# Kernel optimization log

Hardware: AMD Instinct MI355X
Metric: run time of the kernel (lower is better)

The kernel has to match this reference:

```python
import jax, jax.numpy as jnp
import numpy as np

N_NODES = 10000
N_EDGES = 320000
DIM = 256
NUM_HEADS = 8
HEAD_DIM = DIM // NUM_HEADS


def setup_inputs() -> dict:
    key = jax.random.key(0)
    ks = jax.random.split(key, 8)
    s = 1.0 / np.sqrt(DIM)
    x = jax.random.normal(ks[0], (N_NODES, DIM), dtype=jnp.float32)
    src = jax.random.randint(ks[1], (N_EDGES,), 0, N_NODES, dtype=jnp.int32)
    dst = jax.random.randint(ks[2], (N_EDGES,), 0, N_NODES, dtype=jnp.int32)
    Wq = jax.random.normal(ks[3], (DIM, DIM), dtype=jnp.float32) * s
    Wk = jax.random.normal(ks[4], (DIM, DIM), dtype=jnp.float32) * s
    Wv = jax.random.normal(ks[5], (DIM, DIM), dtype=jnp.float32) * s
    Wo = jax.random.normal(ks[6], (DIM, DIM), dtype=jnp.float32) * s
    z = jnp.zeros((DIM,), dtype=jnp.float32)
    return {"x": x, "src": src, "dst": dst,
            "Wq": Wq, "bq": z, "Wk": Wk, "bk": z,
            "Wv": Wv, "bv": z, "Wo": Wo, "bo": z}


def reference(x, src, dst, Wq, bq, Wk, bk, Wv, bv, Wo, bo):
    N = x.shape[0]
    # nn.Linear: y = x @ W.T + b
    q = (x @ Wq.T + bq).reshape(N, NUM_HEADS, HEAD_DIM)
    k = (x @ Wk.T + bk).reshape(N, NUM_HEADS, HEAD_DIM)
    v = (x @ Wv.T + bv).reshape(N, NUM_HEADS, HEAD_DIM)
    # u_dot_v: dot(q[src], k[dst]) per head -> [E, H]
    score = jnp.einsum('ehd,ehd->eh', q[src], k[dst]) / np.sqrt(HEAD_DIM).astype(np.float32)
    # Faithful to source: F.softmax(dim=1) on [E, H, 1] -> softmax over HEADS axis
    attn = jax.nn.softmax(score, axis=1)  # [E, H]
    # u_mul_e then sum-reduce onto destination nodes
    m = v[src] * attn[:, :, None]  # [E, H, HEAD_DIM]
    h = jax.ops.segment_sum(m, dst, num_segments=N).reshape(N, DIM)
    out = h @ Wo.T + bo
    # dropout p=0.0 -> identity
    return out
```

## Files before the change

kernel.cpp:

```cpp
#include <hip/hip_runtime.h>
#include <stdint.h>

#define N_NODES 10000
#define N_EDGES 320000
#define DIM 256
#define NRANGE 4
#define RANGE_DIV 2500
#define PAD_SLOTS 32
#define CNT_STRIDE 16

typedef _Float16 half8 __attribute__((ext_vector_type(8)));
typedef _Float16 half2t __attribute__((ext_vector_type(2)));
typedef float floatx4 __attribute__((ext_vector_type(4)));

#define QK_SCALE 0.17677669529663687f

typedef __attribute__((address_space(3))) uint32_t lds_u32;
typedef __attribute__((address_space(1))) const uint32_t glob_u32;
__device__ __forceinline__ void load16_lds(const _Float16* g, _Float16* l) {
  __builtin_amdgcn_global_load_lds((glob_u32*)g, (lds_u32*)l, 16, 0, 0);
}

__device__ __forceinline__ half8 cvt8s(const float4 a, const float4 b, float sc) {
  half8 o;
  o[0] = (_Float16)(a.x * sc); o[1] = (_Float16)(a.y * sc);
  o[2] = (_Float16)(a.z * sc); o[3] = (_Float16)(a.w * sc);
  o[4] = (_Float16)(b.x * sc); o[5] = (_Float16)(b.y * sc);
  o[6] = (_Float16)(b.z * sc); o[7] = (_Float16)(b.w * sc);
  return o;
}

__global__ void __launch_bounds__(256) prep_k(
    const float* __restrict__ x, const float* __restrict__ Wq,
    const float* __restrict__ Wk, const float* __restrict__ Wv,
    const float* __restrict__ Wo,
    _Float16* __restrict__ xh, _Float16* __restrict__ Wcat,
    _Float16* __restrict__ Woh, int* __restrict__ cntp) {
  int b = blockIdx.x;
  int t = threadIdx.x;
  if (b < 1250) {
    int i = b * 256 + t;
    const float4* p = (const float4*)x;
    ((half8*)xh)[i] = cvt8s(p[2 * i], p[2 * i + 1], 1.0f);
  } else if (b < 1378) {
    int bb = b - 1250;
    int w = bb >> 5;
    int i = (bb & 31) * 256 + t;
    const float* in = (w == 0) ? Wq : (w == 1) ? Wv : (w == 2) ? Wk : Wo;
    _Float16* out = (w < 3) ? (Wcat + (size_t)w * 65536) : Woh;
    float sc = (w == 0) ? QK_SCALE : 1.0f;
    const float4* p = (const float4*)in;
    ((half8*)out)[i] = cvt8s(p[2 * i], p[2 * i + 1], sc);
  } else {
    int idx = (b - 1378) * 256 + t;
#pragma unroll
    for (int k = 0; k < 16; ++k) {
      int j = idx + k * 10240;
      if (j < 160000) ((int4*)cntp)[j] = (int4){0, 0, 0, 0};
    }
  }
}

template <typename STORE>
__device__ __forceinline__ void gemm_tile32(
    _Float16* As, _Float16* Bs,
    const _Float16* __restrict__ A, const _Float16* __restrict__ B,
    int m0, int n0, int t, STORE&& store_fn) {
  int lane = t & 63;
  int wid = t >> 6;
  int l16 = lane & 15;
  int quad = lane >> 4;
  int wm = wid >> 1, wn = wid & 1;

  floatx4 acc[4][4];
#pragma unroll
  for (int i = 0; i < 4; ++i)
#pragma unroll
    for (int j = 0; j < 4; ++j) acc[i][j] = (floatx4){0.f, 0.f, 0.f, 0.f};

  auto stage = [&](int ks, int buf) {
#pragma unroll
    for (int i = 0; i < 2; ++i) {
      int idx = i * 4 + wid;
      int c = idx >> 1;
      int hh2 = idx & 1;
      int r = hh2 * 64 + lane;
      int ar = m0 + r;
      if (ar >= N_NODES) ar = N_NODES - 1;
      load16_lds(A + (size_t)ar * 256 + ks * 32 + c * 8,
                 &As[buf * 4096 + (c * 128 + hh2 * 64) * 8]);
      load16_lds(B + (size_t)(n0 + r) * 256 + ks * 32 + c * 8,
                 &Bs[buf * 4096 + (c * 128 + hh2 * 64) * 8]);
    }
  };

  stage(0, 0);
  __syncthreads();

  for (int ks = 0; ks < 8; ++ks) {
    int bsel = ks & 1;
    if (ks < 7) stage(ks + 1, 1 - bsel);
    half8 af[4], bf[4];
#pragma unroll
    for (int i = 0; i < 4; ++i) {
      af[i] = *(const half8*)&As[bsel * 4096 + (quad * 128 + wm * 64 + i * 16 + l16) * 8];
      bf[i] = *(const half8*)&Bs[bsel * 4096 + (quad * 128 + wn * 64 + i * 16 + l16) * 8];
    }
#pragma unroll
    for (int mi = 0; mi < 4; ++mi)
#pragma unroll
      for (int ni = 0; ni < 4; ++ni)
        acc[mi][ni] =
            __builtin_amdgcn_mfma_f32_16x16x32_f16(af[mi], bf[ni], acc[mi][ni], 0, 0, 0);
    __syncthreads();
  }

#pragma unroll
  for (int mi = 0; mi < 4; ++mi) {
#pragma unroll
    for (int ni = 0; ni < 4; ++ni) {
      int col = n0 + wn * 64 + ni * 16 + l16;
#pragma unroll
      for (int r = 0; r < 4; ++r) {
        int row = m0 + wm * 64 + mi * 16 + quad * 4 + r;
        if (row < N_NODES) store_fn(row, col, acc[mi][ni][r]);
      }
    }
  }
}

__global__ void __launch_bounds__(256) gemm0_scatter_k(
    const _Float16* __restrict__ A, const _Float16* __restrict__ B,
    const float* __restrict__ b0, const float* __restrict__ b1,
    const float* __restrict__ b2,
    _Float16* __restrict__ qv, _Float16* __restrict__ kh,
    const int* __restrict__ src, const int* __restrict__ dst,
    int* __restrict__ cntp, int* __restrict__ slist4) {
  __shared__ _Float16 As[8192];
  __shared__ _Float16 Bs[8192];
  int u = blockIdx.x;
  int t = threadIdx.x;

  if (u >= 474) {
    int e0 = (u - 474) * 582;
    int e1 = e0 + 582;
    if (e1 > N_EDGES) e1 = N_EDGES;
    for (int e = e0 + t; e < e1; e += 256) {
      int s = src[e];
      int r = s / RANGE_DIV;
      int cell = dst[e] * NRANGE + r;
      int pos = atomicAdd(&cntp[(size_t)cell * CNT_STRIDE], 1);
      if (pos < PAD_SLOTS) slist4[cell * PAD_SLOTS + pos] = s;
    }
    return;
  }

  int bx = u % 79, by = u / 79;
  gemm_tile32(As, Bs, A, B, bx * 128, by * 128, t,
              [&](int row, int col, float v) {
                float bias = (col < 256) ? b0[col] * QK_SCALE
                                         : (col < 512) ? b1[col - 256] : b2[col - 512];
                float val = v + bias;
                if (col < 512)
                  qv[(size_t)row * 512 + col] = (_Float16)val;
                else
                  kh[(size_t)row * 256 + (col - 512)] = (_Float16)val;
              });
}

__global__ void __launch_bounds__(256) gemm1_k(
    const _Float16* __restrict__ A, const _Float16* __restrict__ B,
    const float* __restrict__ b0, float* __restrict__ outf) {
  __shared__ _Float16 As[8192];
  __shared__ _Float16 Bs[8192];
  int t = threadIdx.x;
  gemm_tile32(As, Bs, A, B, blockIdx.x * 128, blockIdx.y * 128, t,
              [&](int row, int col, float v) {
                outf[(size_t)row * 256 + col] = v + b0[col];
              });
}

__global__ void __launch_bounds__(256, 4) aggregate_k(
    const _Float16* __restrict__ qv, const _Float16* __restrict__ kh,
    const int* __restrict__ slist4, const int* __restrict__ cntp,
    _Float16* __restrict__ hh) {
  int lane = threadIdx.x & 63;
  int n = blockIdx.x * 4 + (threadIdx.x >> 6);
  if (n >= N_NODES) return;
  int h = lane & 7;
  int g = lane >> 3;

  const int* cb = cntp + (size_t)n * (NRANGE * CNT_STRIDE);
  int d0 = min(cb[0 * CNT_STRIDE], PAD_SLOTS);
  int d1 = min(cb[1 * CNT_STRIDE], PAD_SLOTS);
  int d2 = min(cb[2 * CNT_STRIDE], PAD_SLOTS);
  int d3 = min(cb[3 * CNT_STRIDE], PAD_SLOTS);
  int o1 = d0, o2 = o1 + d1, o3 = o2 + d2;
  int T = o3 + d3;
  const int* nb = slist4 + (size_t)n * (NRANGE * PAD_SLOTS);

  int sidA = 0, sidB = 0;
  {
    int i0 = lane;
    int r0 = (i0 >= o1) + (i0 >= o2) + (i0 >= o3);
    int b0r = (r0 == 0) ? 0 : (r0 == 1) ? o1 : (r0 == 2) ? o2 : o3;
    if (i0 < T) sidA = nb[r0 * PAD_SLOTS + (i0 - b0r)];
    if (T > 64) {
      int i1 = lane + 64;
      int r1 = (i1 >= o1) + (i1 >= o2) + (i1 >= o3);
      int b1r = (r1 == 0) ? 0 : (r1 == 1) ? o1 : (r1 == 2) ? o2 : o3;
      if (i1 < T) sidB = nb[r1 * PAD_SLOTS + (i1 - b1r)];
    }
  }

  half8 kc[4];
  const half8* krow = (const half8*)(kh + (size_t)n * DIM + h * 32);
#pragma unroll
  for (int i = 0; i < 4; ++i) kc[i] = krow[i];
  const half2t* k2 = (const half2t*)kc;

  half2t acc[16];
#pragma unroll
  for (int i = 0; i < 16; ++i) acc[i] = (half2t){(_Float16)0.f, (_Float16)0.f};

  int iters = (T + 7) >> 3;
  if (iters > 0) {
    int s0 = __shfl(sidA, g);
    const half8* rr = (const half8*)(qv + (size_t)s0 * 512 + h * 32);
    half8 qc[4];
#pragma unroll
    for (int i = 0; i < 4; ++i) qc[i] = rr[i];
    bool valid = g < T;

#pragma unroll 1
    for (int jj = 0; jj < iters; ++jj) {
      half8 vc[4];
#pragma unroll
      for (int i = 0; i < 4; ++i) vc[i] = rr[32 + i];
      half8 nq[4];
      bool nvalid = false;
      const half8* nrr = rr;
      if (jj + 1 < iters) {
        int nidx = (jj + 1) * 8 + g;
        int ns = (jj + 1 < 8) ? __shfl(sidA, nidx) : __shfl(sidB, nidx - 64);
        nrr = (const half8*)(qv + (size_t)ns * 512 + h * 32);
#pragma unroll
        for (int i = 0; i < 4; ++i) nq[i] = nrr[i];
        nvalid = nidx < T;
      }
      const half2t* q2 = (const half2t*)qc;
      float pa = 0.f, pb = 0.f, pc = 0.f, pd = 0.f;
#pragma unroll
      for (int i = 0; i < 4; ++i) {
#if __has_builtin(__builtin_amdgcn_fdot2)
        pa = __builtin_amdgcn_fdot2(q2[i], k2[i], pa, false);
        pb = __builtin_amdgcn_fdot2(q2[4 + i], k2[4 + i], pb, false);
        pc = __builtin_amdgcn_fdot2(q2[8 + i], k2[8 + i], pc, false);
        pd = __builtin_amdgcn_fdot2(q2[12 + i], k2[12 + i], pd, false);
#else
        pa += (float)q2[i][0] * (float)k2[i][0] + (float)q2[i][1] * (float)k2[i][1];
        pb += (float)q2[4 + i][0] * (float)k2[4 + i][0] + (float)q2[4 + i][1] * (float)k2[4 + i][1];
        pc += (float)q2[8 + i][0] * (float)k2[8 + i][0] + (float)q2[8 + i][1] * (float)k2[8 + i][1];
        pd += (float)q2[12 + i][0] * (float)k2[12 + i][0] + (float)q2[12 + i][1] * (float)k2[12 + i][1];
#endif
      }
      float p = (pa + pb) + (pc + pd);
      float ex = __expf(p);
      float ssum = ex;
      ssum += __shfl_xor(ssum, 1);
      ssum += __shfl_xor(ssum, 2);
      ssum += __shfl_xor(ssum, 4);
      float a = valid ? (ex * __frcp_rn(ssum)) : 0.f;
      _Float16 ah = (_Float16)a;
      half2t ah2 = (half2t){ah, ah};
      const half2t* v2 = (const half2t*)vc;
#pragma unroll
      for (int i = 0; i < 16; ++i) acc[i] += v2[i] * ah2;
#pragma unroll
      for (int i = 0; i < 4; ++i) qc[i] = nq[i];
      rr = nrr;
      valid = nvalid;
    }
  }

#pragma unroll
  for (int i = 0; i < 16; ++i) {
    union { half2t h2; int v; } u;
    u.h2 = acc[i]; u.v = __shfl_xor(u.v, 8);  acc[i] += u.h2;
    u.h2 = acc[i]; u.v = __shfl_xor(u.v, 16); acc[i] += u.h2;
    u.h2 = acc[i]; u.v = __shfl_xor(u.v, 32); acc[i] += u.h2;
  }
  if (g == 0) {
    half8* hrow = (half8*)(hh + (size_t)n * DIM + h * 32);
    const half8* a8 = (const half8*)acc;
#pragma unroll
    for (int i = 0; i < 4; ++i) hrow[i] = a8[i];
  }
}

extern "C" void kernel_launch(void* const* d_in, const int* in_sizes, int n_in,
                              void* d_out, int out_size, void* d_ws, size_t ws_size,
                              hipStream_t stream) {
  const float* x = (const float*)d_in[0];
  const int* src = (const int*)d_in[1];
  const int* dst = (const int*)d_in[2];
  const float* Wq = (const float*)d_in[3];
  const float* bq = (const float*)d_in[4];
  const float* Wk = (const float*)d_in[5];
  const float* bk = (const float*)d_in[6];
  const float* Wv = (const float*)d_in[7];
  const float* bv = (const float*)d_in[8];
  const float* Wo = (const float*)d_in[9];
  const float* bo = (const float*)d_in[10];

  char* p = (char*)d_ws;
  const size_t SZ_NODE_H = (size_t)N_NODES * DIM * sizeof(_Float16);
  _Float16* xh = (_Float16*)p; p += SZ_NODE_H;
  _Float16* qvv = (_Float16*)p; p += 2 * SZ_NODE_H;
  _Float16* kh = (_Float16*)p; p += SZ_NODE_H;
  _Float16* hh = (_Float16*)p; p += SZ_NODE_H;
  _Float16* Wcat = (_Float16*)p; p += (size_t)768 * 256 * sizeof(_Float16);
  _Float16* Woh = (_Float16*)p; p += (size_t)256 * 256 * sizeof(_Float16);
  int* cntp = (int*)p; p += (size_t)N_NODES * NRANGE * CNT_STRIDE * sizeof(int);
  int* slist4 = (int*)p; p += (size_t)N_NODES * NRANGE * PAD_SLOTS * sizeof(int);

  prep_k<<<1418, 256, 0, stream>>>(x, Wq, Wk, Wv, Wo, xh, Wcat, Woh, cntp);

  gemm0_scatter_k<<<1024, 256, 0, stream>>>(xh, Wcat, bq, bv, bk, qvv, kh,
                                            src, dst, cntp, slist4);

  aggregate_k<<<2500, 256, 0, stream>>>(qvv, kh, slist4, cntp, hh);

  gemm1_k<<<dim3(79, 2), 256, 0, stream>>>(hh, Woh, bo, (float*)d_out);
}
```

Before: 168.9 us.

## Replace LDS-staged GEMM tiles with register-direct per-wave 32x64 MFMA tiles

The shared-memory double-buffered GEMM (global_load_lds plus block barriers) is replaced by a register-only scheme. Each wave loads its A and B fragments straight from global memory and prefetches the next k-step into registers. Tiles shrink from 128x128 per block to 128x64 per block, split as 32x64 per wave, which doubles the block count for both GEMMs and drops barriers and LDS use. The cost is lost operand reuse across waves, since each wave re-reads B from global/L2, and more total global traffic.

```diff
diff --git a/kernel.cpp b/kernel.cpp
--- a/kernel.cpp
+++ b/kernel.cpp
@@ -14,12 +14,6 @@
 typedef float floatx4 __attribute__((ext_vector_type(4)));
 
 #define QK_SCALE 0.17677669529663687f
-
-typedef __attribute__((address_space(3))) uint32_t lds_u32;
-typedef __attribute__((address_space(1))) const uint32_t glob_u32;
-__device__ __forceinline__ void load16_lds(const _Float16* g, _Float16* l) {
-  __builtin_amdgcn_global_load_lds((glob_u32*)g, (lds_u32*)l, 16, 0, 0);
-}
 
 __device__ __forceinline__ half8 cvt8s(const float4 a, const float4 b, float sc) {
   half8 o;
@@ -62,67 +56,64 @@
 }
 
 template <typename STORE>
-__device__ __forceinline__ void gemm_tile32(
-    _Float16* As, _Float16* Bs,
+__device__ __forceinline__ void gemm_reg(
     const _Float16* __restrict__ A, const _Float16* __restrict__ B,
-    int m0, int n0, int t, STORE&& store_fn) {
-  int lane = t & 63;
-  int wid = t >> 6;
+    int m0, int n0, int lane, STORE&& store_fn) {
   int l16 = lane & 15;
   int quad = lane >> 4;
-  int wm = wid >> 1, wn = wid & 1;
-
-  floatx4 acc[4][4];
-#pragma unroll
-  for (int i = 0; i < 4; ++i)
+
+  floatx4 acc[2][4];
+#pragma unroll
+  for (int i = 0; i < 2; ++i)
 #pragma unroll
     for (int j = 0; j < 4; ++j) acc[i][j] = (floatx4){0.f, 0.f, 0.f, 0.f};
 
-  auto stage = [&](int ks, int buf) {
-#pragma unroll
-    for (int i = 0; i < 2; ++i) {
-      int idx = i * 4 + wid;
-      int c = idx >> 1;
-      int hh2 = idx & 1;
-      int r = hh2 * 64 + lane;
-      int ar = m0 + r;
-      if (ar >= N_NODES) ar = N_NODES - 1;
-      load16_lds(A + (size_t)ar * 256 + ks * 32 + c * 8,
-                 &As[buf * 4096 + (c * 128 + hh2 * 64) * 8]);
-      load16_lds(B + (size_t)(n0 + r) * 256 + ks * 32 + c * 8,
-                 &Bs[buf * 4096 + (c * 128 + hh2 * 64) * 8]);
-    }
-  };
-
-  stage(0, 0);
-  __syncthreads();
-
+  const _Float16* ap[2];
+#pragma unroll
+  for (int mi = 0; mi < 2; ++mi) {
+    int r = m0 + mi * 16 + l16;
+    if (r >= N_NODES) r = N_NODES - 1;
+    ap[mi] = A + (size_t)r * 256 + quad * 8;
+  }
+  const _Float16* bp[4];
+#pragma unroll
+  for (int ni = 0; ni < 4; ++ni)
+    bp[ni] = B + (size_t)(n0 + ni * 16 + l16) * 256 + quad * 8;
+
+  half8 a0[2], b0[4], a1[2], b1[4];
+#pragma unroll
+  for (int mi = 0; mi < 2; ++mi) a0[mi] = *(const half8*)(ap[mi]);
+#pragma unroll
+  for (int ni = 0; ni < 4; ++ni) b0[ni] = *(const half8*)(bp[ni]);
+
+#pragma unroll
   for (int ks = 0; ks < 8; ++ks) {
-    int bsel = ks & 1;
-    if (ks < 7) stage(ks + 1, 1 - bsel);
-    half8 af[4], bf[4];
-#pragma unroll
-    for (int i = 0; i < 4; ++i) {
-      af[i] = *(const half8*)&As[bsel * 4096 + (quad * 128 + wm * 64 + i * 16 + l16) * 8];
-      bf[i] = *(const half8*)&Bs[bsel * 4096 + (quad * 128 + wn * 64 + i * 16 + l16) * 8];
-    }
-#pragma unroll
-    for (int mi = 0; mi < 4; ++mi)
+    if (ks < 7) {
+#pragma unroll
+      for (int mi = 0; mi < 2; ++mi) a1[mi] = *(const half8*)(ap[mi] + (ks + 1) * 32);
+#pragma unroll
+      for (int ni = 0; ni < 4; ++ni) b1[ni] = *(const half8*)(bp[ni] + (ks + 1) * 32);
+    }
+#pragma unroll
+    for (int mi = 0; mi < 2; ++mi)
 #pragma unroll
       for (int ni = 0; ni < 4; ++ni)
         acc[mi][ni] =
-            __builtin_amdgcn_mfma_f32_16x16x32_f16(af[mi], bf[ni], acc[mi][ni], 0, 0, 0);
-    __syncthreads();
-  }
-
-#pragma unroll
-  for (int mi = 0; mi < 4; ++mi) {
+            __builtin_amdgcn_mfma_f32_16x16x32_f16(a0[mi], b0[ni], acc[mi][ni], 0, 0, 0);
+#pragma unroll
+    for (int mi = 0; mi < 2; ++mi) a0[mi] = a1[mi];
+#pragma unroll
+    for (int ni = 0; ni < 4; ++ni) b0[ni] = b1[ni];
+  }
+
+#pragma unroll
+  for (int mi = 0; mi < 2; ++mi) {
 #pragma unroll
     for (int ni = 0; ni < 4; ++ni) {
-      int col = n0 + wn * 64 + ni * 16 + l16;
+      int col = n0 + ni * 16 + l16;
 #pragma unroll
       for (int r = 0; r < 4; ++r) {
-        int row = m0 + wm * 64 + mi * 16 + quad * 4 + r;
+        int row = m0 + mi * 16 + quad * 4 + r;
         if (row < N_NODES) store_fn(row, col, acc[mi][ni][r]);
       }
     }
@@ -136,13 +127,11 @@
     _Float16* __restrict__ qv, _Float16* __restrict__ kh,
     const int* __restrict__ src, const int* __restrict__ dst,
     int* __restrict__ cntp, int* __restrict__ slist4) {
-  __shared__ _Float16 As[8192];
-  __shared__ _Float16 Bs[8192];
   int u = blockIdx.x;
   int t = threadIdx.x;
 
-  if (u >= 474) {
-    int e0 = (u - 474) * 582;
+  if (u >= 948) {
+    int e0 = (u - 948) * 582;
     int e1 = e0 + 582;
     if (e1 > N_EDGES) e1 = N_EDGES;
     for (int e = e0 + t; e < e1; e += 256) {
@@ -156,28 +145,31 @@
   }
 
   int bx = u % 79, by = u / 79;
-  gemm_tile32(As, Bs, A, B, bx * 128, by * 128, t,
-              [&](int row, int col, float v) {
-                float bias = (col < 256) ? b0[col] * QK_SCALE
-                                         : (col < 512) ? b1[col - 256] : b2[col - 512];
-                float val = v + bias;
-                if (col < 512)
-                  qv[(size_t)row * 512 + col] = (_Float16)val;
-                else
-                  kh[(size_t)row * 256 + (col - 512)] = (_Float16)val;
-              });
+  int wid = t >> 6, lane = t & 63;
+  int m0 = bx * 128 + wid * 32;
+  int n0 = by * 64;
+  gemm_reg(A, B, m0, n0, lane,
+           [&](int row, int col, float v) {
+             float bias = (col < 256) ? b0[col] * QK_SCALE
+                                      : (col < 512) ? b1[col - 256] : b2[col - 512];
+             float val = v + bias;
+             if (col < 512)
+               qv[(size_t)row * 512 + col] = (_Float16)val;
+             else
+               kh[(size_t)row * 256 + (col - 512)] = (_Float16)val;
+           });
 }
 
 __global__ void __launch_bounds__(256) gemm1_k(
     const _Float16* __restrict__ A, const _Float16* __restrict__ B,
     const float* __restrict__ b0, float* __restrict__ outf) {
-  __shared__ _Float16 As[8192];
-  __shared__ _Float16 Bs[8192];
-  int t = threadIdx.x;
-  gemm_tile32(As, Bs, A, B, blockIdx.x * 128, blockIdx.y * 128, t,
-              [&](int row, int col, float v) {
-                outf[(size_t)row * 256 + col] = v + b0[col];
-              });
+  int u = blockIdx.x;
+  int bx = u % 79, by = u / 79;
+  int wid = threadIdx.x >> 6, lane = threadIdx.x & 63;
+  gemm_reg(A, B, bx * 128 + wid * 32, by * 64, lane,
+           [&](int row, int col, float v) {
+             outf[(size_t)row * 256 + col] = v + b0[col];
+           });
 }
 
 __global__ void __launch_bounds__(256, 4) aggregate_k(
@@ -326,10 +318,10 @@
 
   prep_k<<<1418, 256, 0, stream>>>(x, Wq, Wk, Wv, Wo, xh, Wcat, Woh, cntp);
 
-  gemm0_scatter_k<<<1024, 256, 0, stream>>>(xh, Wcat, bq, bv, bk, qvv, kh,
+  gemm0_scatter_k<<<1498, 256, 0, stream>>>(xh, Wcat, bq, bv, bk, qvv, kh,
                                             src, dst, cntp, slist4);
 
   aggregate_k<<<2500, 256, 0, stream>>>(qvv, kh, slist4, cntp, hh);
 
-  gemm1_k<<<dim3(79, 2), 256, 0, stream>>>(hh, Woh, bo, (float*)d_out);
-}
+  gemm1_k<<<316, 256, 0, stream>>>(hh, Woh, bo, (float*)d_out);
+}
```

After: 171.7 us. About the same (+1.6%).
